# Kernel optimization log

Measured on AMD Instinct MI355X. Metric: run time of the kernel, lower is better.

The kernel has to match this reference:

```python
import jax, jax.numpy as jnp
import numpy as np

B, EH, T = 4, 512, 256
PH, U = 320, 128
JH, NC = 512, 1025


def setup_inputs() -> dict:
    key = jax.random.key(0)
    ks = jax.random.split(key, 8)
    return {
        "enc": jax.random.normal(ks[0], (B, EH, T), dtype=jnp.float32),
        "dec": jax.random.normal(ks[1], (B, PH, U), dtype=jnp.float32),
        "W_enc": jax.random.normal(ks[2], (EH, JH), dtype=jnp.float32) * (EH ** -0.5),
        "b_enc": jax.random.normal(ks[3], (JH,), dtype=jnp.float32) * 0.02,
        "W_pred": jax.random.normal(ks[4], (PH, JH), dtype=jnp.float32) * (PH ** -0.5),
        "b_pred": jax.random.normal(ks[5], (JH,), dtype=jnp.float32) * 0.02,
        "W_out": jax.random.normal(ks[6], (JH, NC), dtype=jnp.float32) * (JH ** -0.5),
        "b_out": jax.random.normal(ks[7], (NC,), dtype=jnp.float32) * 0.02,
    }


def reference(enc, dec, W_enc, b_enc, W_pred, b_pred, W_out, b_out):
    # enc: [B, EH, T] -> transpose -> [B, T, EH]; dec: [B, PH, U] -> [B, U, PH]
    e = jnp.einsum("bht,hj->btj", enc, W_enc) + b_enc        # [B, T, JH]
    p = jnp.einsum("bhu,hj->buj", dec, W_pred) + b_pred      # [B, U, JH]
    h = jax.nn.relu(e[:, :, None, :] + p[:, None, :, :])     # [B, T, U, JH]
    logits = jnp.einsum("btuj,jc->btuc", h, W_out) + b_out   # [B, T, U, NC]
    return jax.nn.log_softmax(logits, axis=-1)
```

## Files before the change

### kernel.cpp

```cpp
#include <hip/hip_runtime.h>
#include <stdint.h>

#define B_  4
#define EH_ 512
#define T_  256
#define PH_ 320
#define U_  128
#define JH_ 512
#define NC_ 1025

typedef __attribute__((ext_vector_type(8))) short short8;
typedef __attribute__((ext_vector_type(4))) short short4v;
typedef __attribute__((ext_vector_type(4))) float floatx4;

__device__ __forceinline__ unsigned short f2bf(float f) {
    unsigned int x = __float_as_uint(f);
    x += 0x7fffu + ((x >> 16) & 1u);
    return (unsigned short)(x >> 16);
}
__device__ __forceinline__ float bf2f(unsigned short u) {
    return __uint_as_float(((unsigned int)u) << 16);
}

__global__ __launch_bounds__(512) void enc_proj(const float* __restrict__ enc,
                                                const float* __restrict__ W_enc,
                                                const float* __restrict__ b_enc,
                                                float* __restrict__ e_out) {
    __shared__ float a_lds[8][EH_];
    const int tid = threadIdx.x;
    const int mb = blockIdx.x * 8;
    const int b  = mb >> 8;
    const int t0 = mb & (T_ - 1);
    {
        const float* src = enc + ((size_t)(b * EH_ + tid) * T_ + t0);
        float4 v0 = *(const float4*)(src);
        float4 v1 = *(const float4*)(src + 4);
        a_lds[0][tid] = v0.x; a_lds[1][tid] = v0.y; a_lds[2][tid] = v0.z; a_lds[3][tid] = v0.w;
        a_lds[4][tid] = v1.x; a_lds[5][tid] = v1.y; a_lds[6][tid] = v1.z; a_lds[7][tid] = v1.w;
    }
    __syncthreads();
    float acc[8];
    const float bias = b_enc[tid];
#pragma unroll
    for (int i = 0; i < 8; i++) acc[i] = bias;
    for (int k4 = 0; k4 < EH_ / 4; k4++) {
        const float w0 = W_enc[(k4 * 4 + 0) * JH_ + tid];
        const float w1 = W_enc[(k4 * 4 + 1) * JH_ + tid];
        const float w2 = W_enc[(k4 * 4 + 2) * JH_ + tid];
        const float w3 = W_enc[(k4 * 4 + 3) * JH_ + tid];
#pragma unroll
        for (int i = 0; i < 8; i++) {
            float4 a = *(const float4*)(&a_lds[i][k4 * 4]);
            acc[i] = fmaf(a.x, w0, acc[i]);
            acc[i] = fmaf(a.y, w1, acc[i]);
            acc[i] = fmaf(a.z, w2, acc[i]);
            acc[i] = fmaf(a.w, w3, acc[i]);
        }
    }
#pragma unroll
    for (int i = 0; i < 8; i++) e_out[(mb + i) * JH_ + tid] = acc[i];
}

__global__ __launch_bounds__(512) void pred_proj(const float* __restrict__ dec,
                                                 const float* __restrict__ W_pred,
                                                 const float* __restrict__ b_pred,
                                                 float* __restrict__ p_out) {
    __shared__ float a_lds[8][PH_];
    const int tid = threadIdx.x;
    const int mb = blockIdx.x * 8;
    const int b  = mb >> 7;
    const int u0 = mb & (U_ - 1);
    if (tid < PH_) {
        const float* src = dec + ((size_t)(b * PH_ + tid) * U_ + u0);
        float4 v0 = *(const float4*)(src);
        float4 v1 = *(const float4*)(src + 4);
        a_lds[0][tid] = v0.x; a_lds[1][tid] = v0.y; a_lds[2][tid] = v0.z; a_lds[3][tid] = v0.w;
        a_lds[4][tid] = v1.x; a_lds[5][tid] = v1.y; a_lds[6][tid] = v1.z; a_lds[7][tid] = v1.w;
    }
    __syncthreads();
    float acc[8];
    const float bias = b_pred[tid];
#pragma unroll
    for (int i = 0; i < 8; i++) acc[i] = bias;
    for (int k4 = 0; k4 < PH_ / 4; k4++) {
        const float w0 = W_pred[(k4 * 4 + 0) * JH_ + tid];
        const float w1 = W_pred[(k4 * 4 + 1) * JH_ + tid];
        const float w2 = W_pred[(k4 * 4 + 2) * JH_ + tid];
        const float w3 = W_pred[(k4 * 4 + 3) * JH_ + tid];
#pragma unroll
        for (int i = 0; i < 8; i++) {
            float4 a = *(const float4*)(&a_lds[i][k4 * 4]);
            acc[i] = fmaf(a.x, w0, acc[i]);
            acc[i] = fmaf(a.y, w1, acc[i]);
            acc[i] = fmaf(a.z, w2, acc[i]);
            acc[i] = fmaf(a.w, w3, acc[i]);
        }
    }
#pragma unroll
    for (int i = 0; i < 8; i++) p_out[(mb + i) * JH_ + tid] = acc[i];
}

__global__ __launch_bounds__(256) void wt_prep(const float* __restrict__ W_out,
                                               unsigned short* __restrict__ WT2) {
    const int idx = blockIdx.x * 256 + threadIdx.x;
    const int k = idx >> 10;
    const int c = idx & 1023;
    const float v = W_out[(size_t)k * NC_ + c];
    const int dst = ((c >> 4) * 16 + (k >> 5)) * 512 +
                    ((k >> 3) & 3) * 128 + (c & 15) * 8 + (k & 7);
    WT2[dst] = f2bf(v);
    if (idx < JH_) WT2[524288 + idx] = f2bf(W_out[(size_t)idx * NC_ + (NC_ - 1)]);
}

__global__ __launch_bounds__(512, 2) void joint_kernel(
        const float* __restrict__ e, const float* __restrict__ p,
        const unsigned short* __restrict__ WT2,
        const float* __restrict__ b_out, float* __restrict__ out) {
    __shared__ __align__(16) char hs_buf[8 * NC_ * 4];
    __shared__ float stripes[8][64];
    __shared__ float rowmax_lds[64];
    __shared__ float lse_lds[64];
    __shared__ float c1024_lds[64];
    unsigned short* h_lds = (unsigned short*)hs_buf;
    float* stage = (float*)hs_buf;

    const int tid = threadIdx.x;
    const int m0 = blockIdx.x * 64;
    const int bb = m0 >> 15;
    const int tt = (m0 >> 7) & (T_ - 1);
    const int u0 = m0 & (U_ - 1);

    const int wave = tid >> 6;
    const int lane = tid & 63;
    const int qd = lane >> 4;
    const int ln = lane & 15;
    const int n0 = wave << 7;

    floatx4 acc[4][8];
#pragma unroll
    for (int i = 0; i < 4; i++)
#pragma unroll
        for (int nt = 0; nt < 8; nt++) acc[i][nt] = (floatx4){0.f, 0.f, 0.f, 0.f};

    const float* e_row = e + (size_t)(bb * T_ + tt) * JH_;
    const float* p_base = p + (size_t)(bb * U_ + u0) * JH_;
    const unsigned short* wt_wave = WT2 + (size_t)wave * 65536 + lane * 8;
    const unsigned short* wt_c1024 = WT2 + 524288;

    float c1024_part = 0.0f;
    const int rr = tid >> 3;
    const int g  = tid & 7;

    const int kq = lane;
    const int rslot = wave;
    unsigned short* h_st = h_lds + rslot * 256 + (((kq >> 1) ^ rslot) * 8) + (kq & 1) * 4;

    for (int ph = 0; ph < 2; ph++) {
        const int kbase = ph * 256;
        const float4 e4 = *(const float4*)(e_row + kbase + kq * 4);
        const float* p_ptr = p_base + (size_t)rslot * JH_ + kbase + kq * 4;
#pragma unroll
        for (int it = 0; it < 8; it++) {
            float4 pv = *(const float4*)(p_ptr + (size_t)it * 8 * JH_);
            short4v hw;
            hw[0] = (short)f2bf(fmaxf(e4.x + pv.x, 0.f));
            hw[1] = (short)f2bf(fmaxf(e4.y + pv.y, 0.f));
            hw[2] = (short)f2bf(fmaxf(e4.z + pv.z, 0.f));
            hw[3] = (short)f2bf(fmaxf(e4.w + pv.w, 0.f));
            *(short4v*)(h_st + it * 8 * 256) = hw;
        }
        __syncthreads();
        for (int ks = 0; ks < 8; ks++) {
            const int k0l = ks * 32;
            const int kb = ph * 8 + ks;
            short8 a[4];
#pragma unroll
            for (int i = 0; i < 4; i++) {
                int m = i * 16 + ln;
                int pc = ((k0l >> 3) + qd) ^ (m & 7);
                a[i] = *(const short8*)(&h_lds[m * 256 + pc * 8]);
            }
#pragma unroll
            for (int nt = 0; nt < 8; nt++) {
                const short8 bfrag = *(const short8*)(wt_wave + (size_t)nt * 8192 + kb * 512);
#pragma unroll
                for (int i = 0; i < 4; i++)
                    acc[i][nt] = __builtin_amdgcn_mfma_f32_16x16x32_bf16(
                            a[i], bfrag, acc[i][nt], 0, 0, 0);
            }
        }
#pragma unroll
        for (int cc = 0; cc < 4; cc++) {
            int c = g * 4 + cc;
            int pc = c ^ (rr & 7);
#pragma unroll
            for (int o = 0; o < 8; o++) {
                c1024_part += bf2f(h_lds[rr * 256 + pc * 8 + o]) *
                              bf2f(wt_c1024[kbase + c * 8 + o]);
            }
        }
        __syncthreads();
    }

    c1024_part += __shfl_down(c1024_part, 4, 8);
    c1024_part += __shfl_down(c1024_part, 2, 8);
    c1024_part += __shfl_down(c1024_part, 1, 8);

#pragma unroll
    for (int nt = 0; nt < 8; nt++) {
        float bv = b_out[n0 + nt * 16 + ln];
#pragma unroll
        for (int i = 0; i < 4; i++) {
            acc[i][nt][0] += bv; acc[i][nt][1] += bv;
            acc[i][nt][2] += bv; acc[i][nt][3] += bv;
        }
    }

    float mx[4][4];
#pragma unroll
    for (int i = 0; i < 4; i++)
#pragma unroll
        for (int r = 0; r < 4; r++) {
            float m = acc[i][0][r];
#pragma unroll
            for (int nt = 1; nt < 8; nt++) m = fmaxf(m, acc[i][nt][r]);
            m = fmaxf(m, __shfl_xor(m, 1, 16));
            m = fmaxf(m, __shfl_xor(m, 2, 16));
            m = fmaxf(m, __shfl_xor(m, 4, 16));
            m = fmaxf(m, __shfl_xor(m, 8, 16));
            mx[i][r] = m;
        }
    if (ln == 0) {
#pragma unroll
        for (int i = 0; i < 4; i++)
#pragma unroll
            for (int r = 0; r < 4; r++)
                stripes[wave][i * 16 + qd * 4 + r] = mx[i][r];
    }
    if (g == 0) c1024_lds[rr] = c1024_part + b_out[NC_ - 1];
    __syncthreads();
    if (tid < 64) {
        float m = c1024_lds[tid];
#pragma unroll
        for (int w = 0; w < 8; w++) m = fmaxf(m, stripes[w][tid]);
        rowmax_lds[tid] = m;
    }
    __syncthreads();

#pragma unroll
    for (int i = 0; i < 4; i++)
#pragma unroll
        for (int r = 0; r < 4; r++) {
            float rm = rowmax_lds[i * 16 + qd * 4 + r];
            float s = 0.f;
#pragma unroll
            for (int nt = 0; nt < 8; nt++) s += __expf(acc[i][nt][r] - rm);
            s += __shfl_xor(s, 1, 16);
            s += __shfl_xor(s, 2, 16);
            s += __shfl_xor(s, 4, 16);
            s += __shfl_xor(s, 8, 16);
            mx[i][r] = s;
        }
    if (ln == 0) {
#pragma unroll
        for (int i = 0; i < 4; i++)
#pragma unroll
            for (int r = 0; r < 4; r++)
                stripes[wave][i * 16 + qd * 4 + r] = mx[i][r];
    }
    __syncthreads();
    if (tid < 64) {
        float rm = rowmax_lds[tid];
        float s = __expf(c1024_lds[tid] - rm);
#pragma unroll
        for (int w = 0; w < 8; w++) s += stripes[w][tid];
        lse_lds[tid] = rm + __logf(s);
    }
    __syncthreads();

#pragma unroll
    for (int c = 0; c < 8; c++) {
        const int i = c >> 1;
        if ((qd >> 1) == (c & 1)) {
#pragma unroll
            for (int r = 0; r < 4; r++) {
                const int lr = (qd & 1) * 4 + r;
                const float l = lse_lds[c * 8 + lr];
#pragma unroll
                for (int nt = 0; nt < 8; nt++)
                    stage[lr * NC_ + n0 + nt * 16 + ln] = acc[i][nt][r] - l;
            }
        }
        if (tid < 8)
            stage[tid * NC_ + 1024] = c1024_lds[c * 8 + tid] - lse_lds[c * 8 + tid];
        __syncthreads();
        const floatx4* src4 = (const floatx4*)stage;
        floatx4* dst4 = (floatx4*)(out + (size_t)(m0 + c * 8) * NC_);
        for (int j = tid; j < (8 * NC_) / 4; j += 512)
            __builtin_nontemporal_store(src4[j], dst4 + j);
        __syncthreads();
    }
}

extern "C" void kernel_launch(void* const* d_in, const int* in_sizes, int n_in,
                              void* d_out, int out_size, void* d_ws, size_t ws_size,
                              hipStream_t stream) {
    const float* enc    = (const float*)d_in[0];
    const float* dec    = (const float*)d_in[1];
    const float* W_enc  = (const float*)d_in[2];
    const float* b_enc  = (const float*)d_in[3];
    const float* W_pred = (const float*)d_in[4];
    const float* b_pred = (const float*)d_in[5];
    const float* W_out  = (const float*)d_in[6];
    const float* b_out  = (const float*)d_in[7];
    float* out = (float*)d_out;

    char* ws = (char*)d_ws;
    float* e_buf = (float*)ws;
    float* p_buf = (float*)(ws + (2u << 20));
    unsigned short* WT2 = (unsigned short*)(ws + (3u << 20));

    enc_proj<<<dim3(128), dim3(512), 0, stream>>>(enc, W_enc, b_enc, e_buf);
    pred_proj<<<dim3(64), dim3(512), 0, stream>>>(dec, W_pred, b_pred, p_buf);
    wt_prep<<<dim3(2048), dim3(256), 0, stream>>>(W_out, WT2);
    joint_kernel<<<dim3(2048), dim3(512), 0, stream>>>(e_buf, p_buf, WT2, b_out, out);
}
```

Measured before the change: 868.9 us.

## Double-buffer joint kernel staging, fuse c1024 column, split-K small projections

The joint kernel now double-buffers the bf16 hidden tile so the second-half h computation and its global loads overlap the first-half MFMA loop. The separate LDS pass for column 1024 is folded into the h-building step as a per-thread FMA accumulation. The output staging is ping-ponged so copy-out of one 8-row chunk overlaps unpacking of the next, which halves the barriers in that loop. The encoder and predictor projections switch to split-K over two thread halves with more blocks to raise parallelism. MFMA sections are also wrapped in s_setprio. In exchange it uses more LDS and more registers, which could reduce occupancy.

```diff
diff --git a/kernel.cpp b/kernel.cpp
--- a/kernel.cpp
+++ b/kernel.cpp
@@ -26,78 +26,100 @@
                                                 const float* __restrict__ W_enc,
                                                 const float* __restrict__ b_enc,
                                                 float* __restrict__ e_out) {
-    __shared__ float a_lds[8][EH_];
+    __shared__ float a_lds[4][EH_];
+    __shared__ float pr[4][JH_];
     const int tid = threadIdx.x;
-    const int mb = blockIdx.x * 8;
+    const int mb = blockIdx.x * 4;
     const int b  = mb >> 8;
     const int t0 = mb & (T_ - 1);
     {
         const float* src = enc + ((size_t)(b * EH_ + tid) * T_ + t0);
         float4 v0 = *(const float4*)(src);
-        float4 v1 = *(const float4*)(src + 4);
         a_lds[0][tid] = v0.x; a_lds[1][tid] = v0.y; a_lds[2][tid] = v0.z; a_lds[3][tid] = v0.w;
-        a_lds[4][tid] = v1.x; a_lds[5][tid] = v1.y; a_lds[6][tid] = v1.z; a_lds[7][tid] = v1.w;
-    }
-    __syncthreads();
-    float acc[8];
-    const float bias = b_enc[tid];
-#pragma unroll
-    for (int i = 0; i < 8; i++) acc[i] = bias;
-    for (int k4 = 0; k4 < EH_ / 4; k4++) {
-        const float w0 = W_enc[(k4 * 4 + 0) * JH_ + tid];
-        const float w1 = W_enc[(k4 * 4 + 1) * JH_ + tid];
-        const float w2 = W_enc[(k4 * 4 + 2) * JH_ + tid];
-        const float w3 = W_enc[(k4 * 4 + 3) * JH_ + tid];
-#pragma unroll
-        for (int i = 0; i < 8; i++) {
-            float4 a = *(const float4*)(&a_lds[i][k4 * 4]);
-            acc[i] = fmaf(a.x, w0, acc[i]);
-            acc[i] = fmaf(a.y, w1, acc[i]);
-            acc[i] = fmaf(a.z, w2, acc[i]);
-            acc[i] = fmaf(a.w, w3, acc[i]);
-        }
-    }
-#pragma unroll
-    for (int i = 0; i < 8; i++) e_out[(mb + i) * JH_ + tid] = acc[i];
+    }
+    __syncthreads();
+    const int j  = tid & 255;
+    const int kh = tid >> 8;
+    const int kbase = kh * 256;
+    float acc[4][2] = {{0.f, 0.f}, {0.f, 0.f}, {0.f, 0.f}, {0.f, 0.f}};
+    for (int k4 = 0; k4 < 64; k4++) {
+        const int k = kbase + k4 * 4;
+        float w00 = W_enc[(k + 0) * JH_ + j], w01 = W_enc[(k + 0) * JH_ + j + 256];
+        float w10 = W_enc[(k + 1) * JH_ + j], w11 = W_enc[(k + 1) * JH_ + j + 256];
+        float w20 = W_enc[(k + 2) * JH_ + j], w21 = W_enc[(k + 2) * JH_ + j + 256];
+        float w30 = W_enc[(k + 3) * JH_ + j], w31 = W_enc[(k + 3) * JH_ + j + 256];
+#pragma unroll
+        for (int i = 0; i < 4; i++) {
+            float4 a = *(const float4*)(&a_lds[i][k]);
+            acc[i][0] = fmaf(a.x, w00, acc[i][0]); acc[i][0] = fmaf(a.y, w10, acc[i][0]);
+            acc[i][0] = fmaf(a.z, w20, acc[i][0]); acc[i][0] = fmaf(a.w, w30, acc[i][0]);
+            acc[i][1] = fmaf(a.x, w01, acc[i][1]); acc[i][1] = fmaf(a.y, w11, acc[i][1]);
+            acc[i][1] = fmaf(a.z, w21, acc[i][1]); acc[i][1] = fmaf(a.w, w31, acc[i][1]);
+        }
+    }
+    if (kh == 1) {
+#pragma unroll
+        for (int i = 0; i < 4; i++) { pr[i][j] = acc[i][0]; pr[i][j + 256] = acc[i][1]; }
+    }
+    __syncthreads();
+    if (kh == 0) {
+        const float b0 = b_enc[j], b1 = b_enc[j + 256];
+#pragma unroll
+        for (int i = 0; i < 4; i++) {
+            e_out[(size_t)(mb + i) * JH_ + j]       = acc[i][0] + pr[i][j] + b0;
+            e_out[(size_t)(mb + i) * JH_ + j + 256] = acc[i][1] + pr[i][j + 256] + b1;
+        }
+    }
 }
 
 __global__ __launch_bounds__(512) void pred_proj(const float* __restrict__ dec,
                                                  const float* __restrict__ W_pred,
                                                  const float* __restrict__ b_pred,
                                                  float* __restrict__ p_out) {
-    __shared__ float a_lds[8][PH_];
+    __shared__ float a_lds[4][PH_];
+    __shared__ float pr[4][JH_];
     const int tid = threadIdx.x;
-    const int mb = blockIdx.x * 8;
+    const int mb = blockIdx.x * 4;
     const int b  = mb >> 7;
     const int u0 = mb & (U_ - 1);
     if (tid < PH_) {
         const float* src = dec + ((size_t)(b * PH_ + tid) * U_ + u0);
         float4 v0 = *(const float4*)(src);
-        float4 v1 = *(const float4*)(src + 4);
         a_lds[0][tid] = v0.x; a_lds[1][tid] = v0.y; a_lds[2][tid] = v0.z; a_lds[3][tid] = v0.w;
-        a_lds[4][tid] = v1.x; a_lds[5][tid] = v1.y; a_lds[6][tid] = v1.z; a_lds[7][tid] = v1.w;
-    }
-    __syncthreads();
-    float acc[8];
-    const float bias = b_pred[tid];
-#pragma unroll
-    for (int i = 0; i < 8; i++) acc[i] = bias;
-    for (int k4 = 0; k4 < PH_ / 4; k4++) {
-        const float w0 = W_pred[(k4 * 4 + 0) * JH_ + tid];
-        const float w1 = W_pred[(k4 * 4 + 1) * JH_ + tid];
-        const float w2 = W_pred[(k4 * 4 + 2) * JH_ + tid];
-        const float w3 = W_pred[(k4 * 4 + 3) * JH_ + tid];
-#pragma unroll
-        for (int i = 0; i < 8; i++) {
-            float4 a = *(const float4*)(&a_lds[i][k4 * 4]);
-            acc[i] = fmaf(a.x, w0, acc[i]);
-            acc[i] = fmaf(a.y, w1, acc[i]);
-            acc[i] = fmaf(a.z, w2, acc[i]);
-            acc[i] = fmaf(a.w, w3, acc[i]);
-        }
-    }
-#pragma unroll
-    for (int i = 0; i < 8; i++) p_out[(mb + i) * JH_ + tid] = acc[i];
+    }
+    __syncthreads();
+    const int j  = tid & 255;
+    const int kh = tid >> 8;
+    const int kbase = kh * 160;
+    float acc[4][2] = {{0.f, 0.f}, {0.f, 0.f}, {0.f, 0.f}, {0.f, 0.f}};
+    for (int k4 = 0; k4 < 40; k4++) {
+        const int k = kbase + k4 * 4;
+        float w00 = W_pred[(k + 0) * JH_ + j], w01 = W_pred[(k + 0) * JH_ + j + 256];
+        float w10 = W_pred[(k + 1) * JH_ + j], w11 = W_pred[(k + 1) * JH_ + j + 256];
+        float w20 = W_pred[(k + 2) * JH_ + j], w21 = W_pred[(k + 2) * JH_ + j + 256];
+        float w30 = W_pred[(k + 3) * JH_ + j], w31 = W_pred[(k + 3) * JH_ + j + 256];
+#pragma unroll
+        for (int i = 0; i < 4; i++) {
+            float4 a = *(const float4*)(&a_lds[i][k]);
+            acc[i][0] = fmaf(a.x, w00, acc[i][0]); acc[i][0] = fmaf(a.y, w10, acc[i][0]);
+            acc[i][0] = fmaf(a.z, w20, acc[i][0]); acc[i][0] = fmaf(a.w, w30, acc[i][0]);
+            acc[i][1] = fmaf(a.x, w01, acc[i][1]); acc[i][1] = fmaf(a.y, w11, acc[i][1]);
+            acc[i][1] = fmaf(a.z, w21, acc[i][1]); acc[i][1] = fmaf(a.w, w31, acc[i][1]);
+        }
+    }
+    if (kh == 1) {
+#pragma unroll
+        for (int i = 0; i < 4; i++) { pr[i][j] = acc[i][0]; pr[i][j + 256] = acc[i][1]; }
+    }
+    __syncthreads();
+    if (kh == 0) {
+        const float b0 = b_pred[j], b1 = b_pred[j + 256];
+#pragma unroll
+        for (int i = 0; i < 4; i++) {
+            p_out[(size_t)(mb + i) * JH_ + j]       = acc[i][0] + pr[i][j] + b0;
+            p_out[(size_t)(mb + i) * JH_ + j + 256] = acc[i][1] + pr[i][j + 256] + b1;
+        }
+    }
 }
 
 __global__ __launch_bounds__(256) void wt_prep(const float* __restrict__ W_out,
@@ -112,17 +134,73 @@
     if (idx < JH_) WT2[524288 + idx] = f2bf(W_out[(size_t)idx * NC_ + (NC_ - 1)]);
 }
 
+__device__ __forceinline__ void kloop(const unsigned short* __restrict__ hb,
+                                      const unsigned short* __restrict__ wt_wave,
+                                      int ph, int ln, int qd,
+                                      floatx4 (&acc)[4][8]) {
+#pragma unroll
+    for (int ks = 0; ks < 8; ks++) {
+        const int k0l = ks * 32;
+        const int kb = ph * 8 + ks;
+        short8 a[4];
+#pragma unroll
+        for (int i = 0; i < 4; i++) {
+            int m = i * 16 + ln;
+            int pc = ((k0l >> 3) + qd) ^ (m & 7);
+            a[i] = *(const short8*)(hb + m * 256 + pc * 8);
+        }
+        __builtin_amdgcn_s_setprio(1);
+#pragma unroll
+        for (int nt = 0; nt < 8; nt++) {
+            const short8 bfrag = *(const short8*)(wt_wave + (size_t)nt * 8192 + kb * 512);
+#pragma unroll
+            for (int i = 0; i < 4; i++)
+                acc[i][nt] = __builtin_amdgcn_mfma_f32_16x16x32_bf16(
+                        a[i], bfrag, acc[i][nt], 0, 0, 0);
+        }
+        __builtin_amdgcn_s_setprio(0);
+    }
+}
+
+__device__ __forceinline__ void stage8(unsigned short* __restrict__ hst,
+                                       const float4 e4, const float4* pv,
+                                       const unsigned short* __restrict__ w1024,
+                                       float* c_acc) {
+    short4v wv = *(const short4v*)(w1024);
+    const float w0 = bf2f((unsigned short)wv[0]);
+    const float w1 = bf2f((unsigned short)wv[1]);
+    const float w2 = bf2f((unsigned short)wv[2]);
+    const float w3 = bf2f((unsigned short)wv[3]);
+#pragma unroll
+    for (int it = 0; it < 8; it++) {
+        float hx = fmaxf(e4.x + pv[it].x, 0.f);
+        float hy = fmaxf(e4.y + pv[it].y, 0.f);
+        float hz = fmaxf(e4.z + pv[it].z, 0.f);
+        float hw_ = fmaxf(e4.w + pv[it].w, 0.f);
+        c_acc[it] = fmaf(hx, w0, c_acc[it]);
+        c_acc[it] = fmaf(hy, w1, c_acc[it]);
+        c_acc[it] = fmaf(hz, w2, c_acc[it]);
+        c_acc[it] = fmaf(hw_, w3, c_acc[it]);
+        short4v hv;
+        hv[0] = (short)f2bf(hx); hv[1] = (short)f2bf(hy);
+        hv[2] = (short)f2bf(hz); hv[3] = (short)f2bf(hw_);
+        *(short4v*)(hst + it * 2048) = hv;
+    }
+}
+
 __global__ __launch_bounds__(512, 2) void joint_kernel(
         const float* __restrict__ e, const float* __restrict__ p,
         const unsigned short* __restrict__ WT2,
         const float* __restrict__ b_out, float* __restrict__ out) {
-    __shared__ __align__(16) char hs_buf[8 * NC_ * 4];
+    __shared__ __align__(16) char hs_buf[65600];
     __shared__ float stripes[8][64];
     __shared__ float rowmax_lds[64];
     __shared__ float lse_lds[64];
     __shared__ float c1024_lds[64];
-    unsigned short* h_lds = (unsigned short*)hs_buf;
-    float* stage = (float*)hs_buf;
+    unsigned short* h0 = (unsigned short*)hs_buf;
+    unsigned short* h1 = (unsigned short*)(hs_buf + 32800);
+    float* s0 = (float*)hs_buf;
+    float* s1 = (float*)(hs_buf + 32800);
 
     const int tid = threadIdx.x;
     const int m0 = blockIdx.x * 64;
@@ -147,72 +225,55 @@
     const unsigned short* wt_wave = WT2 + (size_t)wave * 65536 + lane * 8;
     const unsigned short* wt_c1024 = WT2 + 524288;
 
-    float c1024_part = 0.0f;
-    const int rr = tid >> 3;
-    const int g  = tid & 7;
-
     const int kq = lane;
     const int rslot = wave;
-    unsigned short* h_st = h_lds + rslot * 256 + (((kq >> 1) ^ rslot) * 8) + (kq & 1) * 4;
-
-    for (int ph = 0; ph < 2; ph++) {
-        const int kbase = ph * 256;
-        const float4 e4 = *(const float4*)(e_row + kbase + kq * 4);
-        const float* p_ptr = p_base + (size_t)rslot * JH_ + kbase + kq * 4;
-#pragma unroll
-        for (int it = 0; it < 8; it++) {
-            float4 pv = *(const float4*)(p_ptr + (size_t)it * 8 * JH_);
-            short4v hw;
-            hw[0] = (short)f2bf(fmaxf(e4.x + pv.x, 0.f));
-            hw[1] = (short)f2bf(fmaxf(e4.y + pv.y, 0.f));
-            hw[2] = (short)f2bf(fmaxf(e4.z + pv.z, 0.f));
-            hw[3] = (short)f2bf(fmaxf(e4.w + pv.w, 0.f));
-            *(short4v*)(h_st + it * 8 * 256) = hw;
-        }
-        __syncthreads();
-        for (int ks = 0; ks < 8; ks++) {
-            const int k0l = ks * 32;
-            const int kb = ph * 8 + ks;
-            short8 a[4];
-#pragma unroll
-            for (int i = 0; i < 4; i++) {
-                int m = i * 16 + ln;
-                int pc = ((k0l >> 3) + qd) ^ (m & 7);
-                a[i] = *(const short8*)(&h_lds[m * 256 + pc * 8]);
-            }
-#pragma unroll
-            for (int nt = 0; nt < 8; nt++) {
-                const short8 bfrag = *(const short8*)(wt_wave + (size_t)nt * 8192 + kb * 512);
-#pragma unroll
-                for (int i = 0; i < 4; i++)
-                    acc[i][nt] = __builtin_amdgcn_mfma_f32_16x16x32_bf16(
-                            a[i], bfrag, acc[i][nt], 0, 0, 0);
-            }
-        }
-#pragma unroll
-        for (int cc = 0; cc < 4; cc++) {
-            int c = g * 4 + cc;
-            int pc = c ^ (rr & 7);
-#pragma unroll
-            for (int o = 0; o < 8; o++) {
-                c1024_part += bf2f(h_lds[rr * 256 + pc * 8 + o]) *
-                              bf2f(wt_c1024[kbase + c * 8 + o]);
-            }
-        }
-        __syncthreads();
-    }
-
-    c1024_part += __shfl_down(c1024_part, 4, 8);
-    c1024_part += __shfl_down(c1024_part, 2, 8);
-    c1024_part += __shfl_down(c1024_part, 1, 8);
+    const int hoff = rslot * 256 + (((kq >> 1) ^ rslot) * 8) + (kq & 1) * 4;
+
+    float c_acc[8] = {0.f, 0.f, 0.f, 0.f, 0.f, 0.f, 0.f, 0.f};
+
+    {
+        float4 pva[8];
+        const float* pp = p_base + rslot * JH_ + kq * 4;
+#pragma unroll
+        for (int it = 0; it < 8; it++) pva[it] = *(const float4*)(pp + it * 8 * JH_);
+        const float4 e4a = *(const float4*)(e_row + kq * 4);
+        stage8(h0 + hoff, e4a, pva, wt_c1024 + kq * 4, c_acc);
+    }
+    __syncthreads();
+
+    float4 pvb[8];
+    {
+        const float* pp = p_base + rslot * JH_ + 256 + kq * 4;
+#pragma unroll
+        for (int it = 0; it < 8; it++) pvb[it] = *(const float4*)(pp + it * 8 * JH_);
+    }
+    const float4 e4b = *(const float4*)(e_row + 256 + kq * 4);
+
+    kloop(h0, wt_wave, 0, ln, qd, acc);
+
+    stage8(h1 + hoff, e4b, pvb, wt_c1024 + 256 + kq * 4, c_acc);
+    __syncthreads();
+
+    float brow[8];
+#pragma unroll
+    for (int nt = 0; nt < 8; nt++) brow[nt] = b_out[n0 + nt * 16 + ln];
+
+    kloop(h1, wt_wave, 1, ln, qd, acc);
+
+#pragma unroll
+    for (int it = 0; it < 8; it++) {
+        float v = c_acc[it];
+        v += __shfl_xor(v, 1);  v += __shfl_xor(v, 2);  v += __shfl_xor(v, 4);
+        v += __shfl_xor(v, 8);  v += __shfl_xor(v, 16); v += __shfl_xor(v, 32);
+        if (lane == 0) c1024_lds[it * 8 + wave] = v + b_out[NC_ - 1];
+    }
 
 #pragma unroll
     for (int nt = 0; nt < 8; nt++) {
-        float bv = b_out[n0 + nt * 16 + ln];
-#pragma unroll
-        for (int i = 0; i < 4; i++) {
-            acc[i][nt][0] += bv; acc[i][nt][1] += bv;
-            acc[i][nt][2] += bv; acc[i][nt][3] += bv;
+#pragma unroll
+        for (int i = 0; i < 4; i++) {
+            acc[i][nt][0] += brow[nt]; acc[i][nt][1] += brow[nt];
+            acc[i][nt][2] += brow[nt]; acc[i][nt][3] += brow[nt];
         }
     }
 
@@ -237,7 +298,6 @@
             for (int r = 0; r < 4; r++)
                 stripes[wave][i * 16 + qd * 4 + r] = mx[i][r];
     }
-    if (g == 0) c1024_lds[rr] = c1024_part + b_out[NC_ - 1];
     __syncthreads();
     if (tid < 64) {
         float m = c1024_lds[tid];
@@ -278,28 +338,43 @@
     }
     __syncthreads();
 
-#pragma unroll
-    for (int c = 0; c < 8; c++) {
-        const int i = c >> 1;
-        if ((qd >> 1) == (c & 1)) {
-#pragma unroll
-            for (int r = 0; r < 4; r++) {
-                const int lr = (qd & 1) * 4 + r;
-                const float l = lse_lds[c * 8 + lr];
-#pragma unroll
-                for (int nt = 0; nt < 8; nt++)
-                    stage[lr * NC_ + n0 + nt * 16 + ln] = acc[i][nt][r] - l;
-            }
-        }
-        if (tid < 8)
-            stage[tid * NC_ + 1024] = c1024_lds[c * 8 + tid] - lse_lds[c * 8 + tid];
+#define UNPACK(c, dst)                                                          \
+    {                                                                           \
+        const int i_ = (c) >> 1;                                                \
+        if ((qd >> 1) == ((c) & 1)) {                                           \
+            _Pragma("unroll")                                                   \
+            for (int r = 0; r < 4; r++) {                                       \
+                const int lr = (qd & 1) * 4 + r;                                \
+                const float l = lse_lds[(c) * 8 + lr];                          \
+                _Pragma("unroll")                                               \
+                for (int nt = 0; nt < 8; nt++)                                  \
+                    (dst)[lr * NC_ + n0 + nt * 16 + ln] = acc[i_][nt][r] - l;   \
+            }                                                                   \
+        }                                                                       \
+        if (tid < 8)                                                            \
+            (dst)[tid * NC_ + 1024] = c1024_lds[(c) * 8 + tid] - lse_lds[(c) * 8 + tid]; \
+    }
+#define COPYOUT(c, src)                                                         \
+    {                                                                           \
+        const floatx4* s4_ = (const floatx4*)(src);                             \
+        floatx4* d4_ = (floatx4*)(out + (size_t)(m0 + (c) * 8) * NC_);          \
+        for (int j_ = tid; j_ < 2050; j_ += 512)                                \
+            __builtin_nontemporal_store(s4_[j_], d4_ + j_);                     \
+    }
+
+    UNPACK(0, s0);
+    __syncthreads();
+#pragma unroll
+    for (int c = 1; c < 8; c++) {
+        float* rd = (c & 1) ? s0 : s1;
+        float* wr = (c & 1) ? s1 : s0;
+        COPYOUT(c - 1, rd);
+        UNPACK(c, wr);
         __syncthreads();
-        const floatx4* src4 = (const floatx4*)stage;
-        floatx4* dst4 = (floatx4*)(out + (size_t)(m0 + c * 8) * NC_);
-        for (int j = tid; j < (8 * NC_) / 4; j += 512)
-            __builtin_nontemporal_store(src4[j], dst4 + j);
-        __syncthreads();
-    }
+    }
+    COPYOUT(7, s1);
+#undef UNPACK
+#undef COPYOUT
 }
 
 extern "C" void kernel_launch(void* const* d_in, const int* in_sizes, int n_in,
@@ -320,8 +395,8 @@
     float* p_buf = (float*)(ws + (2u << 20));
     unsigned short* WT2 = (unsigned short*)(ws + (3u << 20));
 
-    enc_proj<<<dim3(128), dim3(512), 0, stream>>>(enc, W_enc, b_enc, e_buf);
-    pred_proj<<<dim3(64), dim3(512), 0, stream>>>(dec, W_pred, b_pred, p_buf);
+    enc_proj<<<dim3(256), dim3(512), 0, stream>>>(enc, W_enc, b_enc, e_buf);
+    pred_proj<<<dim3(128), dim3(512), 0, stream>>>(dec, W_pred, b_pred, p_buf);
     wt_prep<<<dim3(2048), dim3(256), 0, stream>>>(W_out, WT2);
     joint_kernel<<<dim3(2048), dim3(512), 0, stream>>>(e_buf, p_buf, WT2, b_out, out);
 }
```

Result: faster. 788.3 us (-9.3%).
